# Kernel optimization log

Hardware: AMD Instinct MI355X
Metric: run time of the kernel (lower is better)

## Reference

```python
import jax, jax.numpy as jnp
import numpy as np

S, B, C = 7, 2, 20
LC, LN = 5.0, 0.5  # lambda_coord, lambda_noobj
CELL = 1.0 / S


def _iou(b1, b2):
    # center (x, y, w, h) boxes, broadcastable [..., 4]
    x1a, y1a = b1[..., 0] - b1[..., 2] / 2, b1[..., 1] - b1[..., 3] / 2
    x2a, y2a = b1[..., 0] + b1[..., 2] / 2, b1[..., 1] + b1[..., 3] / 2
    x1b, y1b = b2[..., 0] - b2[..., 2] / 2, b2[..., 1] - b2[..., 3] / 2
    x2b, y2b = b2[..., 0] + b2[..., 2] / 2, b2[..., 1] + b2[..., 3] / 2
    iw = jnp.maximum(jnp.minimum(x2a, x2b) - jnp.maximum(x1a, x1b), 0.0)
    ih = jnp.maximum(jnp.minimum(y2a, y2b) - jnp.maximum(y1a, y1b), 0.0)
    inter = iw * ih
    union = b1[..., 2] * b1[..., 3] + b2[..., 2] * b2[..., 3] - inter
    return inter / jnp.maximum(union, 1e-10)


def setup_inputs() -> dict:
    key = jax.random.key(0)
    k1, k2, k3 = jax.random.split(key, 3)
    N, T = 16384, 16
    outputs = jax.random.normal(k1, (N, S, S, B * 5 + C), dtype=jnp.float32)
    # normalized xywh, kept strictly inside (0,1) so grid indices are valid
    boxes = jax.random.uniform(k2, (N, T, 4), dtype=jnp.float32, minval=0.01, maxval=0.99)
    labels = jax.random.randint(k3, (N, T), 1, C + 1)  # class labels in 1..C
    return {"outputs": outputs, "boxes": boxes, "labels": labels}


def reference(outputs, boxes, labels):
    N = outputs.shape[0]
    T = boxes.shape[1]
    bbox = outputs[..., : B * 5].reshape(N, S, S, B, 5)
    conf = bbox[..., 4]                         # [N,S,S,B]
    cls_logits = outputs[..., B * 5:]           # [N,S,S,C]
    # decode predicted centers to absolute image coords (as in the original)
    gx = jnp.arange(S, dtype=outputs.dtype)[None, :, None]  # column index
    gy = jnp.arange(S, dtype=outputs.dtype)[:, None, None]  # row index
    px = (bbox[..., 0] + gx) * CELL
    py = (bbox[..., 1] + gy) * CELL
    pred = jnp.stack([px, py, bbox[..., 2], bbox[..., 3]], axis=-1)  # [N,S,S,B,4]

    tx, ty, tw, th = boxes[..., 0], boxes[..., 1], boxes[..., 2], boxes[..., 3]  # [N,T]
    gxi = (tx * S).astype(jnp.int32)
    gyi = (ty * S).astype(jnp.int32)
    offx = tx * S - gxi.astype(tx.dtype)
    offy = ty * S - gyi.astype(ty.dtype)

    bi = jnp.arange(N)[:, None]  # [N,1] broadcasts with [N,T]
    cell_pred = pred[bi, gyi, gxi]          # [N,T,B,4]
    cell_conf = conf[bi, gyi, gxi]          # [N,T,B]
    cell_cls = cls_logits[bi, gyi, gxi]     # [N,T,C]

    ious = _iou(boxes[:, :, None, :], cell_pred)   # [N,T,B]
    best = (B - 1) - jnp.argmax(ious[..., ::-1], axis=-1)  # [N,T]

    bp = jnp.take_along_axis(cell_pred, best[:, :, None, None], axis=2)[:, :, 0, :]  # [N,T,4]
    bconf = jnp.take_along_axis(cell_conf, best[:, :, None], axis=2)[:, :, 0]        # [N,T]

    eps = 1e-6
    box_loss = (
        (bp[..., 0] - offx) ** 2
        + (bp[..., 1] - offy) ** 2
        + (jnp.sqrt(jnp.maximum(bp[..., 2], eps)) - jnp.sqrt(jnp.maximum(tw, eps))) ** 2
        + (jnp.sqrt(jnp.maximum(bp[..., 3], eps)) - jnp.sqrt(jnp.maximum(th, eps))) ** 2
    ).sum(axis=-1)                                     # [N]
    obj_loss = ((bconf - 1.0) ** 2).sum(axis=-1)        # [N]

    probs = jax.nn.softmax(cell_cls, axis=-1)           # [N,T,C]
    onehot = jax.nn.one_hot(labels - 1, C, dtype=probs.dtype)
    class_loss = ((probs - onehot) ** 2).sum(axis=-1).sum(axis=-1)  # [N]

    obj_mask = jnp.zeros((N, S, S, B), dtype=bool).at[bi, gyi, gxi, best].set(True)
    nm = ~obj_mask
    cnt = nm.sum(axis=(1, 2, 3)).astype(conf.dtype)     # always > 0 (T < S*S*B)
    noobj_loss = (conf ** 2 * nm).sum(axis=(1, 2, 3)) / cnt  # mean over unmasked conf

    per_img = LC * box_loss + class_loss + obj_loss + LN * noobj_loss
    return per_img.mean()
```

## Files before the change

kernel.cpp:

```cpp
#include <hip/hip_runtime.h>

#define NCH   30
#define NCONF 98
#define IMGF  1470
#define IPB   8
#define PAIR4 735
#define LCf 5.0f
#define LNf 0.5f

#define AS1 __attribute__((address_space(1)))
#define AS3 __attribute__((address_space(3)))

__device__ __forceinline__ float img_partial(const float* __restrict__ img,
                                             float4 bx, int lab,
                                             volatile unsigned char* sm,
                                             int lane, int t, int q)
{
    float ns;
    {
        int c = lane >> 1, b = lane & 1;
        float cf = img[c * NCH + b * 5 + 4];
        ns = cf * cf;
        if (lane < NCONF - 64) {
            int s2 = lane + 64;
            int c2 = s2 >> 1, b2 = s2 & 1;
            float cf2 = img[c2 * NCH + b2 * 5 + 4];
            ns += cf2 * cf2;
        }
    }

    const float tx = bx.x, ty = bx.y, tw = bx.z, th = bx.w;
    const float fx = tx * 7.0f, fy = ty * 7.0f;
    const int gxi = (int)fx, gyi = (int)fy;
    const float offx = fx - (float)gxi;
    const float offy = fy - (float)gyi;
    const int cellIdx = gyi * 7 + gxi;
    const float* cell = img + cellIdx * NCH;

    float px = 0.f, py = 0.f, pw = 0.f, ph = 0.f, pc = 0.f, iou_own = 0.f;
    if (q < 2) {
        float rx = cell[q * 5 + 0];
        float ry = cell[q * 5 + 1];
        pw       = cell[q * 5 + 2];
        ph       = cell[q * 5 + 3];
        pc       = cell[q * 5 + 4];
        px = (rx + (float)gxi) * (1.0f / 7.0f);
        py = (ry + (float)gyi) * (1.0f / 7.0f);

        float x1a = tx - tw * 0.5f, y1a = ty - th * 0.5f;
        float x2a = tx + tw * 0.5f, y2a = ty + th * 0.5f;
        float x1b = px - pw * 0.5f, y1b = py - ph * 0.5f;
        float x2b = px + pw * 0.5f, y2b = py + ph * 0.5f;
        float iw = fmaxf(fminf(x2a, x2b) - fmaxf(x1a, x1b), 0.0f);
        float ih = fmaxf(fminf(y2a, y2b) - fmaxf(y1a, y1b), 0.0f);
        float inter = iw * ih;
        float uni = tw * th + pw * ph - inter;
        iou_own = inter / fmaxf(uni, 1e-10f);
    }
    const float iou_other = __shfl_xor(iou_own, 1);
    int bestq = 0;
    if (q < 2) {
        float i0 = (q == 0) ? iou_own   : iou_other;
        float i1 = (q == 0) ? iou_other : iou_own;
        bestq = (i1 >= i0) ? 1 : 0;
    }
    const int best = __shfl(bestq, lane & ~3);
    const int s = cellIdx * 2 + best;

    float contrib = 0.0f;
    const float eps = 1e-6f;
    if (q == best) {
        float dx = px - offx, dy = py - offy;
        float dw = sqrtf(fmaxf(pw, eps)) - sqrtf(fmaxf(tw, eps));
        float dh = sqrtf(fmaxf(ph, eps)) - sqrtf(fmaxf(th, eps));
        float box_l = dx * dx + dy * dy + dw * dw + dh * dh;
        float obj_l = (pc - 1.0f) * (pc - 1.0f);
        contrib = LCf * box_l + obj_l;
    }

    if (q == best) sm[s] = (unsigned char)lane;
    asm volatile("s_waitcnt lgkmcnt(0)" ::: "memory");
    __builtin_amdgcn_sched_barrier(0);
    const bool winner = (q == best) && (sm[s] == (unsigned char)lane);
    const unsigned long long bal = __ballot(winner);
    const int mc = __popcll(bal);
    const float ms = winner ? pc * pc : 0.0f;

    {
        float cv[5];
        #pragma unroll
        for (int i = 0; i < 5; ++i) cv[i] = cell[10 + q * 5 + i];
        float m = fmaxf(fmaxf(fmaxf(cv[0], cv[1]), fmaxf(cv[2], cv[3])), cv[4]);
        m = fmaxf(m, __shfl_xor(m, 1));
        m = fmaxf(m, __shfl_xor(m, 2));
        float esum = 0.f, e2 = 0.f, elab = 0.f;
        #pragma unroll
        for (int i = 0; i < 5; ++i) {
            float e = __expf(cv[i] - m);
            esum += e; e2 += e * e;
            if (q * 5 + i == lab) elab = e;
        }
        esum += __shfl_xor(esum, 1);  esum += __shfl_xor(esum, 2);
        e2   += __shfl_xor(e2,   1);  e2   += __shfl_xor(e2,   2);
        elab += __shfl_xor(elab, 1);  elab += __shfl_xor(elab, 2);
        if (q == 0) {
            float inv = 1.0f / esum;
            contrib += e2 * inv * inv - 2.0f * elab * inv + 1.0f;
        }
    }

    const float invDen = 1.0f / (98.0f - (float)mc);
    return contrib + LNf * (ns - ms) * invDen;
}

__global__ __launch_bounds__(256) void yolo_loss_kernel(
    const float* __restrict__ outputs,
    const float* __restrict__ boxes,
    const int*   __restrict__ labels,
    float*       __restrict__ pair_sum)
{
    const int tid  = threadIdx.x;
    const int wave = tid >> 6;
    const int lane = tid & 63;
    const int t    = lane >> 2;
    const int q    = lane & 3;
    const int n0   = blockIdx.x * IPB + wave * 2;

    __shared__ float         s_buf[IPB * IMGF];
    __shared__ unsigned char s_m[4][2][112];

    const float4* out4 = reinterpret_cast<const float4*>(outputs);
    const size_t pbase = (size_t)(n0 >> 1) * PAIR4;
    char* wbase = (char*)s_buf + (size_t)wave * (PAIR4 * 16);
    #pragma unroll
    for (int k = 0; k < 11; ++k) {
        __builtin_amdgcn_global_load_lds(
            (const AS1 void*)(out4 + pbase + k * 64 + lane),
            (AS3 void*)(wbase + (size_t)k * 64 * 16), 16, 0, 0);
    }
    if (lane < PAIR4 - 704) {
        __builtin_amdgcn_global_load_lds(
            (const AS1 void*)(out4 + pbase + 704 + lane),
            (AS3 void*)(wbase + (size_t)704 * 16), 16, 0, 0);
    }

    const float4* bx4 = reinterpret_cast<const float4*>(boxes);
    const float4 bx0 = bx4[(size_t)n0 * 16 + t];
    const float4 bx1 = bx4[(size_t)(n0 + 1) * 16 + t];
    const int   lab0 = labels[(size_t)n0 * 16 + t] - 1;
    const int   lab1 = labels[(size_t)(n0 + 1) * 16 + t] - 1;

    asm volatile("s_waitcnt vmcnt(0)" ::: "memory");
    __builtin_amdgcn_sched_barrier(0);

    const float* img0 = s_buf + (size_t)wave * 2 * IMGF;
    const float* img1 = img0 + IMGF;

    float v = img_partial(img0, bx0, lab0, s_m[wave][0], lane, t, q)
            + img_partial(img1, bx1, lab1, s_m[wave][1], lane, t, q);

    #pragma unroll
    for (int off = 32; off > 0; off >>= 1) v += __shfl_xor(v, off);
    if (lane == 0) pair_sum[blockIdx.x * 4 + wave] = v;
}

__global__ __launch_bounds__(256) void reduce_mean_kernel(
    const float* __restrict__ pair_sum, float* __restrict__ out, int np, int N)
{
    __shared__ double sd[4];
    double acc = 0.0;
    const float4* p4 = reinterpret_cast<const float4*>(pair_sum);
    for (int i = threadIdx.x; i < np / 4; i += 256) {
        float4 v = p4[i];
        acc += (double)v.x + (double)v.y + (double)v.z + (double)v.w;
    }
    #pragma unroll
    for (int off = 32; off > 0; off >>= 1) acc += __shfl_xor(acc, off);
    if ((threadIdx.x & 63) == 0) sd[threadIdx.x >> 6] = acc;
    __syncthreads();
    if (threadIdx.x == 0)
        out[0] = (float)(((sd[0] + sd[1]) + (sd[2] + sd[3])) / (double)N);
}

extern "C" void kernel_launch(void* const* d_in, const int* in_sizes, int n_in,
                              void* d_out, int out_size, void* d_ws, size_t ws_size,
                              hipStream_t stream) {
    const float* outputs = (const float*)d_in[0];
    const float* boxes   = (const float*)d_in[1];
    const int*   labels  = (const int*)d_in[2];
    float* out = (float*)d_out;

    const int N  = in_sizes[0] / IMGF;
    const int nb = N / IPB;
    const int np = nb * 4;
    float* pair_sum = (float*)d_ws;

    yolo_loss_kernel<<<nb, 256, 0, stream>>>(outputs, boxes, labels, pair_sum);
    reduce_mean_kernel<<<1, 256, 0, stream>>>(pair_sum, out, np, N);
}
```

Measured before the change: 26.69 us.

## Process one image per wave with per-image async LDS loads and block reduction

Changes the work split from two images per wave (8 per block) to one image per wave (4 per block), doubling the grid and halving LDS per block. Because an image is 1470 floats and not 16-byte aligned for odd images, it adds two scalar 4-byte LDS loads plus aligned float4 loads. It also waits partially (vmcnt(2)) so the first confidence values can be read early. Per-block sums are combined in shared memory, so the final reduce reads fewer partials. The aim is more occupancy and latency hiding, at the cost of an extra __syncthreads and some fiddly alignment handling.

```diff
diff --git a/kernel.cpp b/kernel.cpp
--- a/kernel.cpp
+++ b/kernel.cpp
@@ -3,8 +3,6 @@
 #define NCH   30
 #define NCONF 98
 #define IMGF  1470
-#define IPB   8
-#define PAIR4 735
 #define LCf 5.0f
 #define LNf 0.5f
 
@@ -14,19 +12,14 @@
 __device__ __forceinline__ float img_partial(const float* __restrict__ img,
                                              float4 bx, int lab,
                                              volatile unsigned char* sm,
-                                             int lane, int t, int q)
+                                             int lane, int t, int q, float cf1)
 {
-    float ns;
-    {
-        int c = lane >> 1, b = lane & 1;
-        float cf = img[c * NCH + b * 5 + 4];
-        ns = cf * cf;
-        if (lane < NCONF - 64) {
-            int s2 = lane + 64;
-            int c2 = s2 >> 1, b2 = s2 & 1;
-            float cf2 = img[c2 * NCH + b2 * 5 + 4];
-            ns += cf2 * cf2;
-        }
+    float ns = cf1 * cf1;
+    if (lane < NCONF - 64) {
+        int s2 = lane + 64;
+        int c2 = s2 >> 1, b2 = s2 & 1;
+        float cf2 = img[c2 * NCH + b2 * 5 + 4];
+        ns += cf2 * cf2;
     }
 
     const float tx = bx.x, ty = bx.y, tw = bx.z, th = bx.w;
@@ -117,60 +110,73 @@
     const float* __restrict__ outputs,
     const float* __restrict__ boxes,
     const int*   __restrict__ labels,
-    float*       __restrict__ pair_sum)
+    float*       __restrict__ block_sum)
 {
     const int tid  = threadIdx.x;
     const int wave = tid >> 6;
     const int lane = tid & 63;
     const int t    = lane >> 2;
     const int q    = lane & 3;
-    const int n0   = blockIdx.x * IPB + wave * 2;
-
-    __shared__ float         s_buf[IPB * IMGF];
-    __shared__ unsigned char s_m[4][2][112];
-
-    const float4* out4 = reinterpret_cast<const float4*>(outputs);
-    const size_t pbase = (size_t)(n0 >> 1) * PAIR4;
-    char* wbase = (char*)s_buf + (size_t)wave * (PAIR4 * 16);
-    #pragma unroll
-    for (int k = 0; k < 11; ++k) {
-        __builtin_amdgcn_global_load_lds(
-            (const AS1 void*)(out4 + pbase + k * 64 + lane),
-            (AS3 void*)(wbase + (size_t)k * 64 * 16), 16, 0, 0);
-    }
-    if (lane < PAIR4 - 704) {
-        __builtin_amdgcn_global_load_lds(
-            (const AS1 void*)(out4 + pbase + 704 + lane),
-            (AS3 void*)(wbase + (size_t)704 * 16), 16, 0, 0);
-    }
-
-    const float4* bx4 = reinterpret_cast<const float4*>(boxes);
-    const float4 bx0 = bx4[(size_t)n0 * 16 + t];
-    const float4 bx1 = bx4[(size_t)(n0 + 1) * 16 + t];
-    const int   lab0 = labels[(size_t)n0 * 16 + t] - 1;
-    const int   lab1 = labels[(size_t)(n0 + 1) * 16 + t] - 1;
+    const int n    = blockIdx.x * 4 + wave;
+
+    __shared__ float         s_img[4 * IMGF];
+    __shared__ unsigned char s_m[4][112];
+    __shared__ float         s_ws[4];
+
+    const float4 bx = reinterpret_cast<const float4*>(boxes)[(size_t)n * 16 + t];
+    const int   lab = labels[(size_t)n * 16 + t] - 1;
+
+    const float* gsrc = outputs + (size_t)n * IMGF;
+    char* wbase = (char*)&s_img[wave * IMGF];
+    const int odd = wave & 1;
+    {
+        const float* sgp = odd ? gsrc : (gsrc + IMGF - 2);
+        char*        slp = odd ? wbase : (wbase + (size_t)(IMGF - 2) * 4);
+        if (lane < 2) {
+            __builtin_amdgcn_global_load_lds((const AS1 void*)(sgp + lane),
+                                             (AS3 void*)slp, 4, 0, 0);
+        }
+        const float4* g4 = reinterpret_cast<const float4*>(gsrc + (odd ? 2 : 0));
+        char* l4 = wbase + (odd ? 8 : 0);
+        #pragma unroll
+        for (int k = 0; k < 5; ++k) {
+            __builtin_amdgcn_global_load_lds(
+                (const AS1 void*)(g4 + k * 64 + lane),
+                (AS3 void*)(l4 + (size_t)k * 1024), 16, 0, 0);
+        }
+        if (lane < 367 - 320) {
+            __builtin_amdgcn_global_load_lds(
+                (const AS1 void*)(g4 + 320 + lane),
+                (AS3 void*)(l4 + (size_t)5 * 1024), 16, 0, 0);
+        }
+    }
+
+    const float* img = &s_img[wave * IMGF];
+
+    asm volatile("s_waitcnt vmcnt(2)" ::: "memory");
+    __builtin_amdgcn_sched_barrier(0);
+    const float cf1 = img[(lane >> 1) * NCH + (lane & 1) * 5 + 4];
 
     asm volatile("s_waitcnt vmcnt(0)" ::: "memory");
     __builtin_amdgcn_sched_barrier(0);
 
-    const float* img0 = s_buf + (size_t)wave * 2 * IMGF;
-    const float* img1 = img0 + IMGF;
-
-    float v = img_partial(img0, bx0, lab0, s_m[wave][0], lane, t, q)
-            + img_partial(img1, bx1, lab1, s_m[wave][1], lane, t, q);
+    float v = img_partial(img, bx, lab, s_m[wave], lane, t, q, cf1);
 
     #pragma unroll
     for (int off = 32; off > 0; off >>= 1) v += __shfl_xor(v, off);
-    if (lane == 0) pair_sum[blockIdx.x * 4 + wave] = v;
+    if (lane == 0) s_ws[wave] = v;
+    __syncthreads();
+    if (tid == 0)
+        block_sum[blockIdx.x] = (s_ws[0] + s_ws[1]) + (s_ws[2] + s_ws[3]);
 }
 
 __global__ __launch_bounds__(256) void reduce_mean_kernel(
-    const float* __restrict__ pair_sum, float* __restrict__ out, int np, int N)
+    const float* __restrict__ block_sum, float* __restrict__ out, int nb, int N)
 {
     __shared__ double sd[4];
     double acc = 0.0;
-    const float4* p4 = reinterpret_cast<const float4*>(pair_sum);
-    for (int i = threadIdx.x; i < np / 4; i += 256) {
+    const float4* p4 = reinterpret_cast<const float4*>(block_sum);
+    for (int i = threadIdx.x; i < nb / 4; i += 256) {
         float4 v = p4[i];
         acc += (double)v.x + (double)v.y + (double)v.z + (double)v.w;
     }
@@ -191,10 +197,9 @@
     float* out = (float*)d_out;
 
     const int N  = in_sizes[0] / IMGF;
-    const int nb = N / IPB;
-    const int np = nb * 4;
-    float* pair_sum = (float*)d_ws;
-
-    yolo_loss_kernel<<<nb, 256, 0, stream>>>(outputs, boxes, labels, pair_sum);
-    reduce_mean_kernel<<<1, 256, 0, stream>>>(pair_sum, out, np, N);
-}
+    const int nb = N / 4;
+    float* block_sum = (float*)d_ws;
+
+    yolo_loss_kernel<<<nb, 256, 0, stream>>>(outputs, boxes, labels, block_sum);
+    reduce_mean_kernel<<<1, 256, 0, stream>>>(block_sum, out, nb, N);
+}
```

Result: faster. 24.26 us (-9.1%).
